# Optimization experiments

Hardware: AMD Instinct MI355X
Metric: run time of the kernel (lower is better)

## Reference

```python
import jax, jax.numpy as jnp
import numpy as np

B, N, FIN, D1, D2 = 4096, 64, 256, 512, 128
NEG = -10000000.0


def setup_inputs() -> dict:
    key = jax.random.key(0)
    ks = jax.random.split(key, 12)
    s = lambda fan_in: 1.0 / np.sqrt(fan_in)
    return {
        "obs_x": jax.random.normal(ks[0], (B, FIN), jnp.float32),
        "others": jax.random.normal(ks[1], (B, N, FIN), jnp.float32),
        "action_mask": jax.random.randint(ks[2], (B, D2), 0, 2, jnp.int32),
        "W1": jax.random.normal(ks[3], (FIN, D1), jnp.float32) * s(FIN),
        "b1": jnp.zeros((D1,), jnp.float32),
        "W2": jax.random.normal(ks[4], (2 * D1, D2), jnp.float32) * s(2 * D1),
        "b2": jnp.zeros((D2,), jnp.float32),
        "W3": jax.random.normal(ks[5], (2 * D1, D2), jnp.float32) * s(2 * D1),
        "b3": jnp.zeros((D2,), jnp.float32),
        "W4": jax.random.normal(ks[6], (D2, 1), jnp.float32) * s(D2),
        "b4": jnp.zeros((1,), jnp.float32),
    }


def reference(obs_x, others, action_mask, W1, b1, W2, b2, W3, b3, W4, b4):
    # shared fc1 projection of self obs and other agents' obs
    x = obs_x @ W1 + b1                       # [B, D1]
    y = jnp.einsum("bnf,fd->bnd", others, W1) + b1  # [B, N, D1]
    # single-query dot-product attention over other agents
    alpha = jnp.einsum("bd,bnd->bn", x, y) / jnp.sqrt(jnp.float32(x.shape[-1]))
    beta = jax.nn.softmax(alpha, axis=-1)     # [B, N]
    c = jnp.einsum("bn,bnd->bd", beta, y)     # context [B, D1]
    out = jnp.concatenate([x, c], axis=-1)    # [B, 2*D1]
    out1 = jax.nn.softmax(out @ W2 + b2, axis=-1)  # policy branch (softmax then mask, as in source)
    mask = action_mask.astype(out1.dtype)
    logits = out1 + NEG * (1.0 - mask)
    value = (out @ W3 + b3) @ W4 + b4         # [B, 1] value head (stored as self._value_out)
    del value  # forward() returns only the masked logits
    return logits.reshape(-1, D2)
```

## Files before the change

### kernel.cpp

```cpp
#include <hip/hip_runtime.h>
#include <hip/hip_bf16.h>


typedef unsigned short u16;
typedef __bf16 bf16x8 __attribute__((ext_vector_type(8)));
typedef float f32x4 __attribute__((ext_vector_type(4)));

#define FIN 256
#define D1  512
#define D2  128
#define NNA 64
#define NEGV -10000000.0f

__device__ __forceinline__ float bf2f(u16 u) {
  unsigned int i = ((unsigned int)u) << 16;
  return __builtin_bit_cast(float, i);
}
__device__ __forceinline__ u16 f2bf(float f) {
  unsigned int i = __builtin_bit_cast(unsigned int, f);
  return (u16)((i + 0x7FFFu + ((i >> 16) & 1u)) >> 16);
}
__device__ __forceinline__ bf16x8 ld_frag_g(const u16* p) {
  return __builtin_bit_cast(bf16x8, *(const uint4*)p);
}
__device__ __forceinline__ bf16x8 ld_frag_f32(const float* p) {
  float4 a = *(const float4*)p, b = *(const float4*)(p + 4);
  u16 s[8];
  s[0] = f2bf(a.x); s[1] = f2bf(a.y); s[2] = f2bf(a.z); s[3] = f2bf(a.w);
  s[4] = f2bf(b.x); s[5] = f2bf(b.y); s[6] = f2bf(b.z); s[7] = f2bf(b.w);
  return __builtin_bit_cast(bf16x8, *(uint4*)s);
}
__device__ __forceinline__ f32x4 ldnt(const float* p) {
  return __builtin_nontemporal_load((const f32x4*)p);
}

__global__ __launch_bounds__(256) void k_prep(const float* __restrict__ W1,
                                              const float* __restrict__ W2,
                                              u16* __restrict__ W1p,
                                              u16* __restrict__ W2p,
                                              u16* __restrict__ W1tp) {
  int c = blockIdx.x * 256 + threadIdx.x;
  u16 s[8];
  if (c < 16384) {
    int lane = c & 63, nt = (c >> 6) & 31, kt = c >> 11;
    int kb = kt * 32 + (lane >> 4) * 8;
    int n = nt * 16 + (lane & 15);
#pragma unroll
    for (int j = 0; j < 8; ++j) s[j] = f2bf(W1[(kb + j) * D1 + n]);
    *(uint4*)(W1p + c * 8) = *(uint4*)s;
  } else if (c < 20480) {
    int cl = c - 16384;
    int lane = cl & 63, nt = (cl >> 6) & 7, kt = cl >> 9;
    int kb = kt * 32 + (lane >> 4) * 8;
    int n = nt * 16 + (lane & 15);
#pragma unroll
    for (int j = 0; j < 8; ++j) s[j] = f2bf(W2[(kb + j) * D2 + n]);
    *(uint4*)(W2p + cl * 8) = *(uint4*)s;
  } else {
    int cl = c - 20480;
    int lane = cl & 63, nt = (cl >> 6) & 15, kt = cl >> 10;
    int kb = kt * 32 + (lane >> 4) * 8;
    int n = nt * 16 + (lane & 15);
    float4 a = *(const float4*)(W1 + n * D1 + kb);
    float4 b = *(const float4*)(W1 + n * D1 + kb + 4);
    s[0] = f2bf(a.x); s[1] = f2bf(a.y); s[2] = f2bf(a.z); s[3] = f2bf(a.w);
    s[4] = f2bf(b.x); s[5] = f2bf(b.y); s[6] = f2bf(b.z); s[7] = f2bf(b.w);
    *(uint4*)(W1tp + cl * 8) = *(uint4*)s;
  }
}

__global__ __launch_bounds__(512) void k_xz(const float* __restrict__ obs,
                                            const u16* __restrict__ W1p,
                                            const u16* __restrict__ W1tp,
                                            const float* __restrict__ pb1,
                                            u16* __restrict__ outw,
                                            float* __restrict__ zbuf) {
  __shared__ __align__(16) u16 x_s[16 * 520];

  const int tid = threadIdx.x;
  const int w = tid >> 6, lane = tid & 63;
  const int q = lane >> 4, c0 = lane & 15;
  const int m0 = blockIdx.x * 16;

  {
    f32x4 acc[4];
#pragma unroll
    for (int c = 0; c < 4; ++c) acc[c] = (f32x4){0.f, 0.f, 0.f, 0.f};

#pragma unroll 1
    for (int kt = 0; kt < 8; ++kt) {
      bf16x8 afr = ld_frag_f32(obs + (m0 + c0) * FIN + kt * 32 + q * 8);
      bf16x8 bfr[4];
#pragma unroll
      for (int nt = 0; nt < 4; ++nt)
        bfr[nt] = ld_frag_g(W1p + ((kt * 32 + w * 4 + nt) * 64 + lane) * 8);
#pragma unroll
      for (int nt = 0; nt < 4; ++nt)
        acc[nt] = __builtin_amdgcn_mfma_f32_16x16x32_bf16(afr, bfr[nt], acc[nt], 0, 0, 0);
    }

#pragma unroll
    for (int nt = 0; nt < 4; ++nt) {
      const int n = (w * 4 + nt) * 16 + c0;
      const float bias = pb1[n];
#pragma unroll
      for (int i = 0; i < 4; ++i) {
        const int r = q * 4 + i;
        const u16 hv = f2bf(acc[nt][i] + bias);
        outw[(m0 + r) * 512 + n] = hv;
        x_s[r * 520 + n] = hv;
      }
    }
  }
  __syncthreads();

  {
    f32x4 acc[2];
#pragma unroll
    for (int c = 0; c < 2; ++c) acc[c] = (f32x4){0.f, 0.f, 0.f, 0.f};

#pragma unroll 1
    for (int kt = 0; kt < 16; ++kt) {
      bf16x8 afr = __builtin_bit_cast(bf16x8, *(const uint4*)(x_s + c0 * 520 + kt * 32 + q * 8));
      bf16x8 bfr[2];
#pragma unroll
      for (int nt = 0; nt < 2; ++nt)
        bfr[nt] = ld_frag_g(W1tp + ((kt * 16 + w * 2 + nt) * 64 + lane) * 8);
#pragma unroll
      for (int nt = 0; nt < 2; ++nt)
        acc[nt] = __builtin_amdgcn_mfma_f32_16x16x32_bf16(afr, bfr[nt], acc[nt], 0, 0, 0);
    }

#pragma unroll
    for (int nt = 0; nt < 2; ++nt) {
      const int n = (w * 2 + nt) * 16 + c0;
#pragma unroll
      for (int i = 0; i < 4; ++i)
        zbuf[(m0 + q * 4 + i) * 256 + n] = acc[nt][i];
    }
  }
}

__global__ __launch_bounds__(256, 4) void k_attn(const float* __restrict__ others,
                                                 const float* __restrict__ zbuf,
                                                 u16* __restrict__ obarb) {
  __shared__ float s_alpha[64];
  __shared__ float s_beta[64];
  __shared__ float s_part[1024];

  const int tid = threadIdx.x;
  const int b = blockIdx.x;
  const int w = tid >> 6, l = tid & 63;
  const float* src = others + (size_t)b * (NNA * FIN);

  const f32x4 z4 = *(const f32x4*)(zbuf + b * 256 + 4 * l);

  f32x4 o4[16];
#pragma unroll
  for (int r = 0; r < 16; ++r)
    o4[r] = ldnt(src + (w * 16 + r) * 256 + 4 * l);

  float v[16];
#pragma unroll
  for (int r = 0; r < 16; ++r)
    v[r] = o4[r][0] * z4[0] + o4[r][1] * z4[1] + o4[r][2] * z4[2] + o4[r][3] * z4[3];

#pragma unroll
  for (int k = 0; k < 4; ++k) {
    const int m = 1 << k;
    const int half = 8 >> k;
    const bool hi = (l & m) != 0;
#pragma unroll
    for (int i = 0; i < half; ++i) {
      float a = v[i], bv = v[i + half];
      float send = hi ? a : bv;
      float keep = hi ? bv : a;
      v[i] = keep + __shfl_xor(send, m);
    }
  }
  v[0] += __shfl_xor(v[0], 16);
  v[0] += __shfl_xor(v[0], 32);
  const int rr = ((l & 1) << 3) | (((l >> 1) & 1) << 2) | (((l >> 2) & 1) << 1) | ((l >> 3) & 1);
  if (l < 16) s_alpha[w * 16 + rr] = v[0] * 0.04419417382415922f;
  __syncthreads();

  if (tid < 64) {
    float x = s_alpha[tid];
    float mx = x;
#pragma unroll
    for (int off = 1; off < 64; off <<= 1) mx = fmaxf(mx, __shfl_xor(mx, off));
    float e = __expf(x - mx);
    float se = e;
#pragma unroll
    for (int off = 1; off < 64; off <<= 1) se += __shfl_xor(se, off);
    s_beta[tid] = e / se;
  }
  __syncthreads();

  f32x4 p = (f32x4){0.f, 0.f, 0.f, 0.f};
#pragma unroll
  for (int r = 0; r < 16; ++r) {
    const float bb = s_beta[w * 16 + r];
    p[0] += bb * o4[r][0]; p[1] += bb * o4[r][1]; p[2] += bb * o4[r][2]; p[3] += bb * o4[r][3];
  }
  *(f32x4*)(&s_part[w * 256 + 4 * l]) = p;
  __syncthreads();

  const float vv = s_part[tid] + s_part[tid + 256] + s_part[tid + 512] + s_part[tid + 768];
  obarb[(size_t)b * 256 + tid] = f2bf(vv);
}

__global__ __launch_bounds__(256) void k_tail(const u16* __restrict__ outw,
                                              const u16* __restrict__ obarb,
                                              const u16* __restrict__ W1p,
                                              const float* __restrict__ pb1,
                                              const u16* __restrict__ W2p,
                                              const float* __restrict__ pb2,
                                              const int* __restrict__ mask,
                                              float* __restrict__ out) {
  __shared__ __align__(16) u16 c_s[16 * 520];
  __shared__ float s_mx[4][16];
  __shared__ float s_se[4][16];

  const int tid = threadIdx.x;
  const int w = tid >> 6, lane = tid & 63;
  const int q = lane >> 4, c0 = lane & 15;
  const int m0 = blockIdx.x * 16;

  {
    f32x4 acc[8];
#pragma unroll
    for (int c = 0; c < 8; ++c) acc[c] = (f32x4){0.f, 0.f, 0.f, 0.f};

#pragma unroll 1
    for (int kt = 0; kt < 8; ++kt) {
      bf16x8 afr = ld_frag_g(obarb + (m0 + c0) * 256 + kt * 32 + q * 8);
      bf16x8 bfr[8];
#pragma unroll
      for (int nt = 0; nt < 8; ++nt)
        bfr[nt] = ld_frag_g(W1p + ((kt * 32 + w * 8 + nt) * 64 + lane) * 8);
#pragma unroll
      for (int nt = 0; nt < 8; ++nt)
        acc[nt] = __builtin_amdgcn_mfma_f32_16x16x32_bf16(afr, bfr[nt], acc[nt], 0, 0, 0);
    }

#pragma unroll
    for (int nt = 0; nt < 8; ++nt) {
      const int n = (w * 8 + nt) * 16 + c0;
      const float bias = pb1[n];
#pragma unroll
      for (int i = 0; i < 4; ++i)
        c_s[(q * 4 + i) * 520 + n] = f2bf(acc[nt][i] + bias);
    }
  }
  __syncthreads();

  f32x4 acc[2];
#pragma unroll
  for (int c = 0; c < 2; ++c) acc[c] = (f32x4){0.f, 0.f, 0.f, 0.f};

#pragma unroll 1
  for (int kt = 0; kt < 16; ++kt) {
    bf16x8 afr = ld_frag_g(outw + (m0 + c0) * 512 + kt * 32 + q * 8);
    bf16x8 bfr[2];
#pragma unroll
    for (int nt = 0; nt < 2; ++nt)
      bfr[nt] = ld_frag_g(W2p + ((kt * 8 + w * 2 + nt) * 64 + lane) * 8);
#pragma unroll
    for (int nt = 0; nt < 2; ++nt)
      acc[nt] = __builtin_amdgcn_mfma_f32_16x16x32_bf16(afr, bfr[nt], acc[nt], 0, 0, 0);
  }
#pragma unroll 1
  for (int kt = 0; kt < 16; ++kt) {
    bf16x8 afr = __builtin_bit_cast(bf16x8, *(const uint4*)(c_s + c0 * 520 + kt * 32 + q * 8));
    bf16x8 bfr[2];
#pragma unroll
    for (int nt = 0; nt < 2; ++nt)
      bfr[nt] = ld_frag_g(W2p + (((kt + 16) * 8 + w * 2 + nt) * 64 + lane) * 8);
#pragma unroll
    for (int nt = 0; nt < 2; ++nt)
      acc[nt] = __builtin_amdgcn_mfma_f32_16x16x32_bf16(afr, bfr[nt], acc[nt], 0, 0, 0);
  }

  float b2f[2];
#pragma unroll
  for (int nt = 0; nt < 2; ++nt) b2f[nt] = pb2[(w * 2 + nt) * 16 + c0];

  float vv[4][2];
#pragma unroll
  for (int i = 0; i < 4; ++i) {
    float mx = -3.0e38f;
#pragma unroll
    for (int nt = 0; nt < 2; ++nt) { vv[i][nt] = acc[nt][i] + b2f[nt]; mx = fmaxf(mx, vv[i][nt]); }
    mx = fmaxf(mx, __shfl_xor(mx, 1)); mx = fmaxf(mx, __shfl_xor(mx, 2));
    mx = fmaxf(mx, __shfl_xor(mx, 4)); mx = fmaxf(mx, __shfl_xor(mx, 8));
    if (c0 == 0) s_mx[w][q * 4 + i] = mx;
  }
  __syncthreads();

#pragma unroll
  for (int i = 0; i < 4; ++i) {
    const int r = q * 4 + i;
    const float mx = fmaxf(fmaxf(s_mx[0][r], s_mx[1][r]), fmaxf(s_mx[2][r], s_mx[3][r]));
    float se = 0.f;
#pragma unroll
    for (int nt = 0; nt < 2; ++nt) { vv[i][nt] = __expf(vv[i][nt] - mx); se += vv[i][nt]; }
    se += __shfl_xor(se, 1); se += __shfl_xor(se, 2);
    se += __shfl_xor(se, 4); se += __shfl_xor(se, 8);
    if (c0 == 0) s_se[w][q * 4 + i] = se;
  }
  __syncthreads();

#pragma unroll
  for (int i = 0; i < 4; ++i) {
    const int r = q * 4 + i;
    const int row = m0 + r;
    const float inv = 1.f / (s_se[0][r] + s_se[1][r] + s_se[2][r] + s_se[3][r]);
#pragma unroll
    for (int nt = 0; nt < 2; ++nt) {
      const int col = (w * 2 + nt) * 16 + c0;
      float p = fminf(fmaxf(vv[i][nt] * inv, 0.f), 1.f);
      float o = mask[row * D2 + col] ? p : (p + NEGV);
      out[row * D2 + col] = o;
    }
  }
}

extern "C" void kernel_launch(void* const* d_in, const int* in_sizes, int n_in,
                              void* d_out, int out_size, void* d_ws, size_t ws_size,
                              hipStream_t stream) {
  const float* obs = (const float*)d_in[0];
  const float* oth = (const float*)d_in[1];
  const int*   msk = (const int*)d_in[2];
  const float* W1  = (const float*)d_in[3];
  const float* b1  = (const float*)d_in[4];
  const float* W2  = (const float*)d_in[5];
  const float* b2  = (const float*)d_in[6];
  float* out = (float*)d_out;

  char* ws = (char*)d_ws;
  u16*   W1p   = (u16*)ws;
  u16*   W2p   = (u16*)(ws + 262144);
  u16*   W1tp  = (u16*)(ws + 327680);
  u16*   outw  = (u16*)(ws + 589824);
  float* zbuf  = (float*)(ws + 4784128);
  u16*   obarb = (u16*)(ws + 8978432);

  k_prep<<<144, 256, 0, stream>>>(W1, W2, W1p, W2p, W1tp);
  k_xz<<<256, 512, 0, stream>>>(obs, W1p, W1tp, b1, outw, zbuf);
  k_attn<<<4096, 256, 0, stream>>>(oth, zbuf, obarb);
  k_tail<<<256, 256, 0, stream>>>(outw, obarb, W1p, b1, W2p, b2, msk, out);
}
```

Baseline: 389.2 us.

## Fuse projection, attention and policy-head kernels into one per-16-row kernel

Merges the x/z projection, the per-row attention and the tail GEMM plus softmax into a single kernel. Each block of 256 threads handles 16 batch rows. Intermediates (x, z, the attention context and c) now stay in shared memory instead of going through global workspace buffers, which removes two kernel launches and their global round-trips. In exchange, the attention stage over the large `others` tensor drops from 4096 blocks to 256 blocks, each looping serially over 16 rows with barriers between steps. That cuts memory-level parallelism and occupancy on the dominant bandwidth-bound phase.

After: 384.8 us. About the same (-1.1%).

```diff
diff --git a/kernel.cpp b/kernel.cpp
--- a/kernel.cpp
+++ b/kernel.cpp
@@ -69,13 +69,25 @@
   }
 }
 
-__global__ __launch_bounds__(512) void k_xz(const float* __restrict__ obs,
-                                            const u16* __restrict__ W1p,
-                                            const u16* __restrict__ W1tp,
-                                            const float* __restrict__ pb1,
-                                            u16* __restrict__ outw,
-                                            float* __restrict__ zbuf) {
-  __shared__ __align__(16) u16 x_s[16 * 520];
+__global__ __launch_bounds__(256) void k_all(const float* __restrict__ obs,
+                                             const float* __restrict__ others,
+                                             const u16* __restrict__ W1p,
+                                             const u16* __restrict__ W1tp,
+                                             const u16* __restrict__ W2p,
+                                             const float* __restrict__ pb1,
+                                             const float* __restrict__ pb2,
+                                             const int* __restrict__ mask,
+                                             float* __restrict__ out) {
+  __shared__ __align__(16) char pool[46848];
+  u16*   x_s     = (u16*)pool;
+  float* z_s     = (float*)(pool + 16640);
+  u16*   c_s     = (u16*)(pool + 16640);
+  u16*   obar_s  = (u16*)(pool + 33280);
+  float* s_alpha = (float*)(pool + 41728);
+  float* s_beta  = (float*)(pool + 41984);
+  float* s_part  = (float*)(pool + 42240);
+  float* s_mx    = (float*)(pool + 46336);
+  float* s_se    = (float*)(pool + 46592);
 
   const int tid = threadIdx.x;
   const int w = tid >> 6, lane = tid & 63;
@@ -83,158 +95,13 @@
   const int m0 = blockIdx.x * 16;
 
   {
-    f32x4 acc[4];
-#pragma unroll
-    for (int c = 0; c < 4; ++c) acc[c] = (f32x4){0.f, 0.f, 0.f, 0.f};
+    f32x4 acc[8];
+#pragma unroll
+    for (int c = 0; c < 8; ++c) acc[c] = (f32x4){0.f, 0.f, 0.f, 0.f};
 
 #pragma unroll 1
     for (int kt = 0; kt < 8; ++kt) {
       bf16x8 afr = ld_frag_f32(obs + (m0 + c0) * FIN + kt * 32 + q * 8);
-      bf16x8 bfr[4];
-#pragma unroll
-      for (int nt = 0; nt < 4; ++nt)
-        bfr[nt] = ld_frag_g(W1p + ((kt * 32 + w * 4 + nt) * 64 + lane) * 8);
-#pragma unroll
-      for (int nt = 0; nt < 4; ++nt)
-        acc[nt] = __builtin_amdgcn_mfma_f32_16x16x32_bf16(afr, bfr[nt], acc[nt], 0, 0, 0);
-    }
-
-#pragma unroll
-    for (int nt = 0; nt < 4; ++nt) {
-      const int n = (w * 4 + nt) * 16 + c0;
-      const float bias = pb1[n];
-#pragma unroll
-      for (int i = 0; i < 4; ++i) {
-        const int r = q * 4 + i;
-        const u16 hv = f2bf(acc[nt][i] + bias);
-        outw[(m0 + r) * 512 + n] = hv;
-        x_s[r * 520 + n] = hv;
-      }
-    }
-  }
-  __syncthreads();
-
-  {
-    f32x4 acc[2];
-#pragma unroll
-    for (int c = 0; c < 2; ++c) acc[c] = (f32x4){0.f, 0.f, 0.f, 0.f};
-
-#pragma unroll 1
-    for (int kt = 0; kt < 16; ++kt) {
-      bf16x8 afr = __builtin_bit_cast(bf16x8, *(const uint4*)(x_s + c0 * 520 + kt * 32 + q * 8));
-      bf16x8 bfr[2];
-#pragma unroll
-      for (int nt = 0; nt < 2; ++nt)
-        bfr[nt] = ld_frag_g(W1tp + ((kt * 16 + w * 2 + nt) * 64 + lane) * 8);
-#pragma unroll
-      for (int nt = 0; nt < 2; ++nt)
-        acc[nt] = __builtin_amdgcn_mfma_f32_16x16x32_bf16(afr, bfr[nt], acc[nt], 0, 0, 0);
-    }
-
-#pragma unroll
-    for (int nt = 0; nt < 2; ++nt) {
-      const int n = (w * 2 + nt) * 16 + c0;
-#pragma unroll
-      for (int i = 0; i < 4; ++i)
-        zbuf[(m0 + q * 4 + i) * 256 + n] = acc[nt][i];
-    }
-  }
-}
-
-__global__ __launch_bounds__(256, 4) void k_attn(const float* __restrict__ others,
-                                                 const float* __restrict__ zbuf,
-                                                 u16* __restrict__ obarb) {
-  __shared__ float s_alpha[64];
-  __shared__ float s_beta[64];
-  __shared__ float s_part[1024];
-
-  const int tid = threadIdx.x;
-  const int b = blockIdx.x;
-  const int w = tid >> 6, l = tid & 63;
-  const float* src = others + (size_t)b * (NNA * FIN);
-
-  const f32x4 z4 = *(const f32x4*)(zbuf + b * 256 + 4 * l);
-
-  f32x4 o4[16];
-#pragma unroll
-  for (int r = 0; r < 16; ++r)
-    o4[r] = ldnt(src + (w * 16 + r) * 256 + 4 * l);
-
-  float v[16];
-#pragma unroll
-  for (int r = 0; r < 16; ++r)
-    v[r] = o4[r][0] * z4[0] + o4[r][1] * z4[1] + o4[r][2] * z4[2] + o4[r][3] * z4[3];
-
-#pragma unroll
-  for (int k = 0; k < 4; ++k) {
-    const int m = 1 << k;
-    const int half = 8 >> k;
-    const bool hi = (l & m) != 0;
-#pragma unroll
-    for (int i = 0; i < half; ++i) {
-      float a = v[i], bv = v[i + half];
-      float send = hi ? a : bv;
-      float keep = hi ? bv : a;
-      v[i] = keep + __shfl_xor(send, m);
-    }
-  }
-  v[0] += __shfl_xor(v[0], 16);
-  v[0] += __shfl_xor(v[0], 32);
-  const int rr = ((l & 1) << 3) | (((l >> 1) & 1) << 2) | (((l >> 2) & 1) << 1) | ((l >> 3) & 1);
-  if (l < 16) s_alpha[w * 16 + rr] = v[0] * 0.04419417382415922f;
-  __syncthreads();
-
-  if (tid < 64) {
-    float x = s_alpha[tid];
-    float mx = x;
-#pragma unroll
-    for (int off = 1; off < 64; off <<= 1) mx = fmaxf(mx, __shfl_xor(mx, off));
-    float e = __expf(x - mx);
-    float se = e;
-#pragma unroll
-    for (int off = 1; off < 64; off <<= 1) se += __shfl_xor(se, off);
-    s_beta[tid] = e / se;
-  }
-  __syncthreads();
-
-  f32x4 p = (f32x4){0.f, 0.f, 0.f, 0.f};
-#pragma unroll
-  for (int r = 0; r < 16; ++r) {
-    const float bb = s_beta[w * 16 + r];
-    p[0] += bb * o4[r][0]; p[1] += bb * o4[r][1]; p[2] += bb * o4[r][2]; p[3] += bb * o4[r][3];
-  }
-  *(f32x4*)(&s_part[w * 256 + 4 * l]) = p;
-  __syncthreads();
-
-  const float vv = s_part[tid] + s_part[tid + 256] + s_part[tid + 512] + s_part[tid + 768];
-  obarb[(size_t)b * 256 + tid] = f2bf(vv);
-}
-
-__global__ __launch_bounds__(256) void k_tail(const u16* __restrict__ outw,
-                                              const u16* __restrict__ obarb,
-                                              const u16* __restrict__ W1p,
-                                              const float* __restrict__ pb1,
-                                              const u16* __restrict__ W2p,
-                                              const float* __restrict__ pb2,
-                                              const int* __restrict__ mask,
-                                              float* __restrict__ out) {
-  __shared__ __align__(16) u16 c_s[16 * 520];
-  __shared__ float s_mx[4][16];
-  __shared__ float s_se[4][16];
-
-  const int tid = threadIdx.x;
-  const int w = tid >> 6, lane = tid & 63;
-  const int q = lane >> 4, c0 = lane & 15;
-  const int m0 = blockIdx.x * 16;
-
-  {
-    f32x4 acc[8];
-#pragma unroll
-    for (int c = 0; c < 8; ++c) acc[c] = (f32x4){0.f, 0.f, 0.f, 0.f};
-
-#pragma unroll 1
-    for (int kt = 0; kt < 8; ++kt) {
-      bf16x8 afr = ld_frag_g(obarb + (m0 + c0) * 256 + kt * 32 + q * 8);
       bf16x8 bfr[8];
 #pragma unroll
       for (int nt = 0; nt < 8; ++nt)
@@ -250,6 +117,124 @@
       const float bias = pb1[n];
 #pragma unroll
       for (int i = 0; i < 4; ++i)
+        x_s[(q * 4 + i) * 520 + n] = f2bf(acc[nt][i] + bias);
+    }
+  }
+  __syncthreads();
+
+  {
+    f32x4 acc[4];
+#pragma unroll
+    for (int c = 0; c < 4; ++c) acc[c] = (f32x4){0.f, 0.f, 0.f, 0.f};
+
+#pragma unroll 1
+    for (int kt = 0; kt < 16; ++kt) {
+      bf16x8 afr = __builtin_bit_cast(bf16x8, *(const uint4*)(x_s + c0 * 520 + kt * 32 + q * 8));
+      bf16x8 bfr[4];
+#pragma unroll
+      for (int nt = 0; nt < 4; ++nt)
+        bfr[nt] = ld_frag_g(W1tp + ((kt * 16 + w * 4 + nt) * 64 + lane) * 8);
+#pragma unroll
+      for (int nt = 0; nt < 4; ++nt)
+        acc[nt] = __builtin_amdgcn_mfma_f32_16x16x32_bf16(afr, bfr[nt], acc[nt], 0, 0, 0);
+    }
+
+#pragma unroll
+    for (int nt = 0; nt < 4; ++nt) {
+      const int n = (w * 4 + nt) * 16 + c0;
+#pragma unroll
+      for (int i = 0; i < 4; ++i)
+        z_s[(q * 4 + i) * 256 + n] = acc[nt][i];
+    }
+  }
+  __syncthreads();
+
+#pragma unroll 1
+  for (int bi = 0; bi < 16; ++bi) {
+    const float* src = others + (size_t)(m0 + bi) * (NNA * FIN);
+    const f32x4 z4 = *(const f32x4*)(z_s + bi * 256 + 4 * lane);
+
+    f32x4 o4[16];
+#pragma unroll
+    for (int r = 0; r < 16; ++r)
+      o4[r] = ldnt(src + (w * 16 + r) * 256 + 4 * lane);
+
+    float v[16];
+#pragma unroll
+    for (int r = 0; r < 16; ++r)
+      v[r] = o4[r][0] * z4[0] + o4[r][1] * z4[1] + o4[r][2] * z4[2] + o4[r][3] * z4[3];
+
+#pragma unroll
+    for (int k = 0; k < 4; ++k) {
+      const int m = 1 << k;
+      const int half = 8 >> k;
+      const bool hi = (lane & m) != 0;
+#pragma unroll
+      for (int i = 0; i < half; ++i) {
+        float a = v[i], bv = v[i + half];
+        float send = hi ? a : bv;
+        float keep = hi ? bv : a;
+        v[i] = keep + __shfl_xor(send, m);
+      }
+    }
+    v[0] += __shfl_xor(v[0], 16);
+    v[0] += __shfl_xor(v[0], 32);
+    const int rr = ((lane & 1) << 3) | (((lane >> 1) & 1) << 2) |
+                   (((lane >> 2) & 1) << 1) | ((lane >> 3) & 1);
+    if (lane < 16) s_alpha[w * 16 + rr] = v[0] * 0.04419417382415922f;
+    __syncthreads();
+
+    if (tid < 64) {
+      float x = s_alpha[tid];
+      float mx = x;
+#pragma unroll
+      for (int off = 1; off < 64; off <<= 1) mx = fmaxf(mx, __shfl_xor(mx, off));
+      float e = __expf(x - mx);
+      float se = e;
+#pragma unroll
+      for (int off = 1; off < 64; off <<= 1) se += __shfl_xor(se, off);
+      s_beta[tid] = e / se;
+    }
+    __syncthreads();
+
+    f32x4 p = (f32x4){0.f, 0.f, 0.f, 0.f};
+#pragma unroll
+    for (int r = 0; r < 16; ++r) {
+      const float bb = s_beta[w * 16 + r];
+      p[0] += bb * o4[r][0]; p[1] += bb * o4[r][1];
+      p[2] += bb * o4[r][2]; p[3] += bb * o4[r][3];
+    }
+    *(f32x4*)(&s_part[w * 256 + 4 * lane]) = p;
+    __syncthreads();
+
+    const float vv = s_part[tid] + s_part[tid + 256] + s_part[tid + 512] + s_part[tid + 768];
+    obar_s[bi * 264 + tid] = f2bf(vv);
+  }
+  __syncthreads();
+
+  {
+    f32x4 acc[8];
+#pragma unroll
+    for (int c = 0; c < 8; ++c) acc[c] = (f32x4){0.f, 0.f, 0.f, 0.f};
+
+#pragma unroll 1
+    for (int kt = 0; kt < 8; ++kt) {
+      bf16x8 afr = __builtin_bit_cast(bf16x8, *(const uint4*)(obar_s + c0 * 264 + kt * 32 + q * 8));
+      bf16x8 bfr[8];
+#pragma unroll
+      for (int nt = 0; nt < 8; ++nt)
+        bfr[nt] = ld_frag_g(W1p + ((kt * 32 + w * 8 + nt) * 64 + lane) * 8);
+#pragma unroll
+      for (int nt = 0; nt < 8; ++nt)
+        acc[nt] = __builtin_amdgcn_mfma_f32_16x16x32_bf16(afr, bfr[nt], acc[nt], 0, 0, 0);
+    }
+
+#pragma unroll
+    for (int nt = 0; nt < 8; ++nt) {
+      const int n = (w * 8 + nt) * 16 + c0;
+      const float bias = pb1[n];
+#pragma unroll
+      for (int i = 0; i < 4; ++i)
         c_s[(q * 4 + i) * 520 + n] = f2bf(acc[nt][i] + bias);
     }
   }
@@ -261,7 +246,7 @@
 
 #pragma unroll 1
   for (int kt = 0; kt < 16; ++kt) {
-    bf16x8 afr = ld_frag_g(outw + (m0 + c0) * 512 + kt * 32 + q * 8);
+    bf16x8 afr = __builtin_bit_cast(bf16x8, *(const uint4*)(x_s + c0 * 520 + kt * 32 + q * 8));
     bf16x8 bfr[2];
 #pragma unroll
     for (int nt = 0; nt < 2; ++nt)
@@ -294,20 +279,20 @@
     for (int nt = 0; nt < 2; ++nt) { vv[i][nt] = acc[nt][i] + b2f[nt]; mx = fmaxf(mx, vv[i][nt]); }
     mx = fmaxf(mx, __shfl_xor(mx, 1)); mx = fmaxf(mx, __shfl_xor(mx, 2));
     mx = fmaxf(mx, __shfl_xor(mx, 4)); mx = fmaxf(mx, __shfl_xor(mx, 8));
-    if (c0 == 0) s_mx[w][q * 4 + i] = mx;
+    if (c0 == 0) s_mx[w * 16 + q * 4 + i] = mx;
   }
   __syncthreads();
 
 #pragma unroll
   for (int i = 0; i < 4; ++i) {
     const int r = q * 4 + i;
-    const float mx = fmaxf(fmaxf(s_mx[0][r], s_mx[1][r]), fmaxf(s_mx[2][r], s_mx[3][r]));
+    const float mx = fmaxf(fmaxf(s_mx[r], s_mx[16 + r]), fmaxf(s_mx[32 + r], s_mx[48 + r]));
     float se = 0.f;
 #pragma unroll
     for (int nt = 0; nt < 2; ++nt) { vv[i][nt] = __expf(vv[i][nt] - mx); se += vv[i][nt]; }
     se += __shfl_xor(se, 1); se += __shfl_xor(se, 2);
     se += __shfl_xor(se, 4); se += __shfl_xor(se, 8);
-    if (c0 == 0) s_se[w][q * 4 + i] = se;
+    if (c0 == 0) s_se[w * 16 + q * 4 + i] = se;
   }
   __syncthreads();
 
@@ -315,7 +300,7 @@
   for (int i = 0; i < 4; ++i) {
     const int r = q * 4 + i;
     const int row = m0 + r;
-    const float inv = 1.f / (s_se[0][r] + s_se[1][r] + s_se[2][r] + s_se[3][r]);
+    const float inv = 1.f / (s_se[r] + s_se[16 + r] + s_se[32 + r] + s_se[48 + r]);
 #pragma unroll
     for (int nt = 0; nt < 2; ++nt) {
       const int col = (w * 2 + nt) * 16 + c0;
@@ -339,15 +324,10 @@
   float* out = (float*)d_out;
 
   char* ws = (char*)d_ws;
-  u16*   W1p   = (u16*)ws;
-  u16*   W2p   = (u16*)(ws + 262144);
-  u16*   W1tp  = (u16*)(ws + 327680);
-  u16*   outw  = (u16*)(ws + 589824);
-  float* zbuf  = (float*)(ws + 4784128);
-  u16*   obarb = (u16*)(ws + 8978432);
+  u16* W1p  = (u16*)ws;
+  u16* W2p  = (u16*)(ws + 262144);
+  u16* W1tp = (u16*)(ws + 327680);
 
   k_prep<<<144, 256, 0, stream>>>(W1, W2, W1p, W2p, W1tp);
-  k_xz<<<256, 512, 0, stream>>>(obs, W1p, W1tp, b1, outw, zbuf);
-  k_attn<<<4096, 256, 0, stream>>>(oth, zbuf, obarb);
-  k_tail<<<256, 256, 0, stream>>>(outw, obarb, W1p, b1, W2p, b2, msk, out);
-}
+  k_all<<<256, 256, 0, stream>>>(obs, oth, W1p, W1tp, W2p, b1, b2, msk, out);
+}
```
